# Performance work log

Measured on AMD Instinct MI355X. Metric: run time of the kernel, lower is better.

The kernel has to match this reference:

```python
import jax, jax.numpy as jnp
import numpy as np

N_HEAD = 8
D_HEAD = 128   # dim_k = dim_q = dim_v
SEG_LEN = 512
EPS = 1e-6


def setup_inputs() -> dict:
    key = jax.random.key(0)
    ks = jax.random.split(key, 8)
    B, T, D = 2, 4096, 1024
    scale = 0.02
    x = jax.random.normal(ks[0], (B, T, D), dtype=jnp.float32)
    w_q = jax.random.normal(ks[1], (D, N_HEAD * D_HEAD), dtype=jnp.float32) * scale
    w_k = jax.random.normal(ks[2], (D, N_HEAD * D_HEAD), dtype=jnp.float32) * scale
    w_v = jax.random.normal(ks[3], (D, N_HEAD * D_HEAD), dtype=jnp.float32) * scale
    b_q = jnp.zeros((N_HEAD * D_HEAD,), jnp.float32)
    b_k = jnp.zeros((N_HEAD * D_HEAD,), jnp.float32)
    b_v = jnp.zeros((N_HEAD * D_HEAD,), jnp.float32)
    beta = jnp.zeros((N_HEAD,), jnp.float32)
    return {"x": x, "w_q": w_q, "b_q": b_q, "w_k": w_k, "b_k": b_k,
            "w_v": w_v, "b_v": b_v, "beta": beta}


def _heads(y, B, T):
    # [B,T,H*D] -> [B,H,T,D]
    return y.reshape(B, T, N_HEAD, D_HEAD).transpose(0, 2, 1, 3)


def reference(x, w_q, b_q, w_k, b_k, w_v, b_v, beta):
    B, T, _ = x.shape
    S = T // SEG_LEN
    q = _heads(x @ w_q + b_q, B, T)
    k = _heads(x @ w_k + b_k, B, T)
    v = _heads(x @ w_v + b_v, B, T)

    # segment: [B,H,T,D] -> [S,B,H,L,D]
    def seg(y):
        return y.reshape(B, N_HEAD, S, SEG_LEN, D_HEAD).transpose(2, 0, 1, 3, 4)
    qs, ks_, vs = seg(q), seg(k), seg(v)

    causal = jnp.tril(jnp.ones((SEG_LEN, SEG_LEN), bool))
    gate = jax.nn.sigmoid(beta).reshape(1, N_HEAD, 1, 1)
    inv_sqrt_d = 1.0 / jnp.sqrt(jnp.asarray(D_HEAD, x.dtype))

    def step(carry, segdat):
        M, z = carry                      # M: [B,H,Dk,Dv], z: [B,H,Dk]
        qc, kc, vc = segdat               # [B,H,L,D]
        sq = jax.nn.elu(qc) + 1.0
        sk = jax.nn.elu(kc) + 1.0
        # retrieval from memory BEFORE update
        a_mem = jnp.einsum('bhld,bhde->bhle', sq, M) / (
            jnp.einsum('bhld,bhd->bhl', sq, z)[..., None] + EPS)
        # delta-rule memory update
        retr_k = jnp.einsum('bhld,bhde->bhle', sk, M) / (
            jnp.einsum('bhld,bhd->bhl', sk, z)[..., None] + EPS)
        M = M + jnp.einsum('bhld,bhle->bhde', sk, vc - retr_k)
        z = z + sk.sum(axis=2)
        # local causal dot-product attention within the segment
        scores = jnp.einsum('bhld,bhmd->bhlm', qc, kc) * inv_sqrt_d
        scores = jnp.where(causal, scores, jnp.asarray(-1e30, scores.dtype))
        a_dot = jnp.einsum('bhlm,bhmd->bhld', jax.nn.softmax(scores, axis=-1), vc)
        # long-term context injection
        a = gate * a_mem + (1.0 - gate) * a_dot
        return (M, z), a

    M0 = jnp.zeros((B, N_HEAD, D_HEAD, D_HEAD), x.dtype)
    z0 = jnp.zeros((B, N_HEAD, D_HEAD), x.dtype)
    _, out = jax.lax.scan(step, (M0, z0), (qs, ks_, vs))
    # [S,B,H,L,D] -> [B,T,H*D]
    out = out.transpose(1, 3, 0, 2, 4).reshape(B, T, N_HEAD * D_HEAD)
    # wait: axes of out are [S,B,H,L,D]; reorder to [B,S,L,H,D]
    return out


# fix ordering: define reference properly (overrides above draft path)
def reference(x, w_q, b_q, w_k, b_k, w_v, b_v, beta):
    B, T, _ = x.shape
    S = T // SEG_LEN
    q = _heads(x @ w_q + b_q, B, T)
    k = _heads(x @ w_k + b_k, B, T)
    v = _heads(x @ w_v + b_v, B, T)

    def seg(y):
        return y.reshape(B, N_HEAD, S, SEG_LEN, D_HEAD).transpose(2, 0, 1, 3, 4)
    qs, ks_, vs = seg(q), seg(k), seg(v)

    causal = jnp.tril(jnp.ones((SEG_LEN, SEG_LEN), bool))
    gate = jax.nn.sigmoid(beta).reshape(1, N_HEAD, 1, 1)
    inv_sqrt_d = 1.0 / jnp.sqrt(jnp.asarray(D_HEAD, x.dtype))

    def step(carry, segdat):
        M, z = carry
        qc, kc, vc = segdat
        sq = jax.nn.elu(qc) + 1.0
        sk = jax.nn.elu(kc) + 1.0
        a_mem = jnp.einsum('bhld,bhde->bhle', sq, M) / (
            jnp.einsum('bhld,bhd->bhl', sq, z)[..., None] + EPS)
        retr_k = jnp.einsum('bhld,bhde->bhle', sk, M) / (
            jnp.einsum('bhld,bhd->bhl', sk, z)[..., None] + EPS)
        M = M + jnp.einsum('bhld,bhle->bhde', sk, vc - retr_k)
        z = z + sk.sum(axis=2)
        scores = jnp.einsum('bhld,bhmd->bhlm', qc, kc) * inv_sqrt_d
        scores = jnp.where(causal, scores, jnp.asarray(-1e30, scores.dtype))
        a_dot = jnp.einsum('bhlm,bhmd->bhld', jax.nn.softmax(scores, axis=-1), vc)
        a = gate * a_mem + (1.0 - gate) * a_dot
        return (M, z), a

    M0 = jnp.zeros((B, N_HEAD, D_HEAD, D_HEAD), x.dtype)
    z0 = jnp.zeros((B, N_HEAD, D_HEAD), x.dtype)
    _, out = jax.lax.scan(step, (M0, z0), (qs, ks_, vs))  # [S,B,H,L,D]
    out = out.transpose(1, 0, 3, 2, 4).reshape(B, T, N_HEAD * D_HEAD)
    return out
```

## Files before the change

kernel.cpp:

```cpp
#include <hip/hip_runtime.h>
#include <hip/hip_bf16.h>

typedef __attribute__((ext_vector_type(8))) short bf16x8;
typedef __attribute__((ext_vector_type(4))) float f32x4;
typedef unsigned short u16;
typedef unsigned int u32;

#define DEV static __device__ __forceinline__

DEV float bf2f(u16 u){ u32 x = ((u32)u)<<16; float f; __builtin_memcpy(&f,&x,4); return f; }
DEV u16 f2bf(float f){ u32 x; __builtin_memcpy(&x,&f,4); return (u16)((x + 0x7fffu + ((x>>16)&1u))>>16); }
DEV float elu1(float x){ return x > 0.f ? x + 1.f : __expf(x); }

DEV void gload16(const u16* g, u16* l){
  __builtin_amdgcn_global_load_lds(
      (const __attribute__((address_space(1))) unsigned int*)(g),
      (__attribute__((address_space(3))) unsigned int*)(l), 16, 0, 0);
}

#define MFMA(a,b,c) __builtin_amdgcn_mfma_f32_16x16x32_bf16((a),(b),(c),0,0,0)

#define NB 2
#define NT 4096
#define NH 8
#define DH 128
#define NS 8
#define SL 512
#define ND 1024
#define N3 3072
#define EPS 1e-6f

__global__ __launch_bounds__(256) void k_xc(const float* __restrict__ x, u16* __restrict__ xb){
  int i = blockIdx.x*256 + threadIdx.x;
  const float4 v0 = *(const float4*)(x + (size_t)i*8);
  const float4 v1 = *(const float4*)(x + (size_t)i*8 + 4);
  bf16x8 o;
  o[0]=(short)f2bf(v0.x); o[1]=(short)f2bf(v0.y); o[2]=(short)f2bf(v0.z); o[3]=(short)f2bf(v0.w);
  o[4]=(short)f2bf(v1.x); o[5]=(short)f2bf(v1.y); o[6]=(short)f2bf(v1.z); o[7]=(short)f2bf(v1.w);
  *(bf16x8*)(xb + (size_t)i*8) = o;
}

__global__ __launch_bounds__(256) void k_wt(const float* __restrict__ wq,
                                            const float* __restrict__ wk,
                                            const float* __restrict__ wv,
                                            u16* __restrict__ wt,
                                            float* __restrict__ cs){
  __shared__ float t[32][33];
  const int z = blockIdx.z;
  const float* w = (z==0) ? wq : (z==1 ? wk : wv);
  const int k0 = blockIdx.x*32, n0 = blockIdx.y*32;
  const int tx = threadIdx.x, ty = threadIdx.y;
  if (z==0 && blockIdx.x==0 && blockIdx.y==0){
    const int tid = ty*32 + tx;
#pragma unroll
    for (int i=0;i<64;i++) cs[tid + i*256] = 0.f;
  }
#pragma unroll
  for (int i=0;i<4;i++) t[ty+i*8][tx] = w[(size_t)(k0+ty+i*8)*ND + n0+tx];
  __syncthreads();
#pragma unroll
  for (int i=0;i<4;i++)
    wt[(size_t)(z*ND + n0+ty+i*8)*ND + k0+tx] = f2bf(t[tx][ty+i*8]);
}

__global__ __launch_bounds__(256) void k_gemm(const u16* __restrict__ xb,
                                              const u16* __restrict__ wt,
                                              const float* __restrict__ bq,
                                              const float* __restrict__ bk,
                                              const float* __restrict__ bv,
                                              u16* __restrict__ qkv,
                                              u16* __restrict__ pkTo,
                                              u16* __restrict__ vto,
                                              float* __restrict__ cs){
  __shared__ __align__(16) u16 As[2][128*64];
  __shared__ __align__(16) u16 Bs[2][128*64];
  const int m0 = blockIdx.x*128, n0 = blockIdx.y*128;
  const int tid = threadIdx.x;
  const int w = tid>>6, lane = tid&63, g = lane>>4, li = lane&15;
  const int wr = w>>1, wc = w&1;
  const int srow = lane>>3;
  const int ssl  = (lane&7) ^ srow;
  f32x4 z4 = {0.f,0.f,0.f,0.f};
  f32x4 acc[4][4];
#pragma unroll
  for (int mi=0;mi<4;mi++)
#pragma unroll
    for (int ni=0;ni<4;ni++) acc[mi][ni] = z4;

#define STAGE(kt_) do{                                                          \
    const int k0_ = (kt_)*64;                                                   \
    u16* A_ = (u16*)As[(kt_)&1];                                                \
    u16* B_ = (u16*)Bs[(kt_)&1];                                                \
    _Pragma("unroll")                                                           \
    for (int i_=0;i_<4;i_++){                                                   \
      const int c_ = i_*4 + w;                                                  \
      const int row_ = c_*8 + srow;                                             \
      gload16(xb + (size_t)(m0+row_)*ND + k0_ + ssl*8, A_ + c_*512);            \
      gload16(wt + (size_t)(n0+row_)*ND + k0_ + ssl*8, B_ + c_*512);            \
    }                                                                           \
  }while(0)

  STAGE(0);
  for (int kt=0; kt<16; ++kt){
    if (kt < 15){ STAGE(kt+1); asm volatile("s_waitcnt vmcnt(8)" ::: "memory"); }
    else        {              asm volatile("s_waitcnt vmcnt(0)" ::: "memory"); }
    __builtin_amdgcn_s_barrier();
    __builtin_amdgcn_sched_barrier(0);
    const u16* Ab = (const u16*)As[kt&1];
    const u16* Bb = (const u16*)Bs[kt&1];
#pragma unroll
    for (int kk=0;kk<2;kk++){
      bf16x8 a[4], bb[4];
#pragma unroll
      for (int mi=0;mi<4;mi++){
        int row = wr*64 + mi*16 + li;
        int slot = kk*4 + g;
        a[mi] = *(const bf16x8*)(Ab + row*64 + ((slot^(row&7))<<3));
      }
#pragma unroll
      for (int ni=0;ni<4;ni++){
        int row = wc*64 + ni*16 + li;
        int slot = kk*4 + g;
        bb[ni] = *(const bf16x8*)(Bb + row*64 + ((slot^(row&7))<<3));
      }
#pragma unroll
      for (int mi=0;mi<4;mi++)
#pragma unroll
        for (int ni=0;ni<4;ni++)
          acc[mi][ni] = MFMA(a[mi], bb[ni], acc[mi][ni]);
    }
    __builtin_amdgcn_sched_barrier(0);
    __builtin_amdgcn_s_barrier();
    __builtin_amdgcn_sched_barrier(0);
  }
#undef STAGE

  const int part = n0 >> 10;
  const int hh = (n0 >> 7) & 7;
  const int bb2 = m0 >> 12;
  const int tloc = m0 & (NT-1);
  const int rb = lane>>3, cb = lane&7;
  u16* SCw = (w < 2 ? (u16*)As[0] : (u16*)Bs[0]) + (w&1)*4096;

  if (part < 2){
#pragma unroll
    for (int ni=0;ni<4;ni++){
      const int n = n0 + wc*64 + ni*16 + li;
      const float bias = (part==0) ? bq[n] : bk[n-ND];
#pragma unroll
      for (int mi=0;mi<4;mi++)
#pragma unroll
        for (int rr=0;rr<4;rr++){
          const int ml = mi*16 + 4*g + rr;
          const int nl = ni*16 + li;
          SCw[ml*64 + (((nl>>3)^(ml&7))<<3) + (nl&7)] = f2bf(acc[mi][ni][rr] + bias);
        }
    }
    __syncthreads();
#pragma unroll
    for (int j=0;j<8;j++){
      const int r = j*8 + rb;
      bf16x8 v = *(const bf16x8*)(SCw + r*64 + ((cb^(r&7))<<3));
      *(bf16x8*)(qkv + (size_t)(m0 + wr*64 + r)*N3 + n0 + wc*64 + cb*8) = v;
    }
  }
  if (part >= 1){
    __syncthreads();
    float csum[4] = {0.f,0.f,0.f,0.f};
#pragma unroll
    for (int ni=0;ni<4;ni++){
      const int n = n0 + wc*64 + ni*16 + li;
      const float bias = (part==1) ? bk[n-ND] : bv[n-2*ND];
      const int nl = ni*16 + li;
#pragma unroll
      for (int mi=0;mi<4;mi++){
        float v0 = acc[mi][ni][0] + bias;
        float v1 = acc[mi][ni][1] + bias;
        float v2 = acc[mi][ni][2] + bias;
        float v3 = acc[mi][ni][3] + bias;
        if (part==1){
          v0 = elu1(v0); v1 = elu1(v1); v2 = elu1(v2); v3 = elu1(v3);
          csum[ni] += v0+v1+v2+v3;
        }
        short4 pk;
        pk.x = (short)f2bf(v0); pk.y = (short)f2bf(v1);
        pk.z = (short)f2bf(v2); pk.w = (short)f2bf(v3);
        const int gran = (2*mi + (g>>1)) ^ (nl&7);
        *(short4*)(SCw + nl*64 + (gran<<3) + 4*(g&1)) = pk;
      }
    }
    __syncthreads();
    u16* dstT = (part==1) ? pkTo : vto;
    const int bh = bb2*8 + hh;
#pragma unroll
    for (int j=0;j<8;j++){
      const int r = j*8 + rb;
      bf16x8 v = *(const bf16x8*)(SCw + r*64 + ((cb^(r&7))<<3));
      *(bf16x8*)(dstT + (size_t)(bh*DH + wc*64 + r)*NT + tloc + wr*64 + cb*8) = v;
    }
    if (part==1){
      const int s = tloc >> 9;
      const int bhs = bb2*64 + hh*8 + s;
#pragma unroll
      for (int ni=0;ni<4;ni++){
        float c = csum[ni];
        c += __shfl_xor(c,16); c += __shfl_xor(c,32);
        if (g==0)
          atomicAdd(&cs[(size_t)bhs*DH + wc*64 + ni*16 + li], c);
      }
    }
  }
}

__global__ __launch_bounds__(512) void k_dinv(const u16* __restrict__ qkv,
                                              const float* __restrict__ cs,
                                              float* __restrict__ dinvK){
  const int bhs = blockIdx.x, half = blockIdx.y;
  const int b = bhs>>6, h = (bhs>>3)&7, s = bhs&7;
  const int tid = threadIdx.x, w = tid>>6, lane = tid&63, grp = lane>>4, li = lane&15;
  __shared__ float zl[128];
  if (tid < 128){
    float a = 0.f;
    for (int sp=0; sp<s; ++sp) a += cs[(size_t)(bhs - s + sp)*DH + tid];
    zl[tid] = a;
  }
  __syncthreads();
#pragma unroll
  for (int it=0; it<8; ++it){
    const int r = half*256 + w*32 + it*4 + grp;
    bf16x8 v = *(const bf16x8*)(qkv + (size_t)(b*NT + s*SL + r)*N3 + ND + h*DH + li*8);
    float p = 0.f;
#pragma unroll
    for (int j=0;j<8;j++) p += elu1(bf2f((u16)v[j])) * zl[li*8+j];
    p += __shfl_xor(p,1); p += __shfl_xor(p,2);
    p += __shfl_xor(p,4); p += __shfl_xor(p,8);
    if (li == 0) dinvK[(size_t)bhs*SL + r] = 1.f/(p + EPS);
  }
}

__global__ __launch_bounds__(512) void k_gram(const u16* __restrict__ pkT,
                                              const u16* __restrict__ vtb,
                                              const float* __restrict__ dinvK,
                                              u16* __restrict__ G, float* __restrict__ Bm){
  const int bhs = blockIdx.x, ec = blockIdx.y;
  const int bh = bhs>>3, s = bhs&7, tb = s*SL;
  const int tid = threadIdx.x, w = tid>>6, lane = tid&63, g = lane>>4, li = lane&15;
  __shared__ __align__(16) u16 Bk[32*512];
  __shared__ __align__(16) u16 Bv[32*512];
  __shared__ float dv[512];
  dv[tid] = dinvK[(size_t)bhs*SL + tid];
#pragma unroll
  for (int i=0;i<4;i++){
    const int ee = i*8 + w;
    const size_t rowo = ((size_t)bh*DH + ec*32 + ee)*NT + tb + ((lane^w)<<3);
    gload16(pkT + rowo, Bk + ee*512);
    gload16(vtb + rowo, Bv + ee*512);
  }
  __syncthreads();
  f32x4 z4 = {0.f,0.f,0.f,0.f};
  f32x4 Ga[2] = {z4,z4}, Ba[2] = {z4,z4};
  const u16* arow = pkT + ((size_t)bh*DH + 16*w + li)*NT + tb;
  for (int ks=0; ks<16; ++ks){
    const int r0 = ks*32 + g*8;
    bf16x8 araw = *(const bf16x8*)(arow + r0);
    float4 d0 = *(const float4*)(dv + r0);
    float4 d1 = *(const float4*)(dv + r0 + 4);
    bf16x8 ascl;
    ascl[0] = (short)f2bf(bf2f((u16)araw[0]) * d0.x);
    ascl[1] = (short)f2bf(bf2f((u16)araw[1]) * d0.y);
    ascl[2] = (short)f2bf(bf2f((u16)araw[2]) * d0.z);
    ascl[3] = (short)f2bf(bf2f((u16)araw[3]) * d0.w);
    ascl[4] = (short)f2bf(bf2f((u16)araw[4]) * d1.x);
    ascl[5] = (short)f2bf(bf2f((u16)araw[5]) * d1.y);
    ascl[6] = (short)f2bf(bf2f((u16)araw[6]) * d1.z);
    ascl[7] = (short)f2bf(bf2f((u16)araw[7]) * d1.w);
    const int slot = ks*4 + g;
#pragma unroll
    for (int ni=0;ni<2;ni++){
      const int ee = ni*16 + li;
      bf16x8 bk8 = *(const bf16x8*)(Bk + ee*512 + ((slot^(li&7))<<3));
      bf16x8 bv8 = *(const bf16x8*)(Bv + ee*512 + ((slot^(li&7))<<3));
      Ga[ni] = MFMA(ascl, bk8, Ga[ni]);
      Ba[ni] = MFMA(araw, bv8, Ba[ni]);
    }
  }
#pragma unroll
  for (int ni=0;ni<2;ni++)
#pragma unroll
    for (int rr=0;rr<4;rr++){
      const int dd = 16*w + 4*g + rr;
      const int ee = ec*32 + ni*16 + li;
      G[((size_t)bhs*DH + dd)*DH + ee] = f2bf(Ga[ni][rr]);
      Bm[((size_t)bhs*DH + dd)*DH + ee] = Ba[ni][rr];
    }
}

__global__ __launch_bounds__(512) void k_scan(const u16* __restrict__ G,
                                              const float* __restrict__ Bm,
                                              u16* __restrict__ MTs){
  const int bh = blockIdx.x, ec = blockIdx.y;
  const int tid = threadIdx.x, w = tid>>6, lane = tid&63, g = lane>>4, li = lane&15;
  __shared__ float MF[16*132];
  __shared__ __align__(16) u16 MB[16*128];
  for (int i = tid; i < 16*132; i += 512) MF[i] = 0.f;
  __syncthreads();
  const int dr = w*16 + li;
  for (int s=0;s<NS;s++){
    const size_t bhs = (size_t)bh*NS + s;
    if (tid < 256){
      const int e = tid>>4, dg = tid&15;
      const float* src = MF + e*132 + dg*8;
      bf16x8 v;
#pragma unroll
      for (int j=0;j<8;j++) v[j] = (short)f2bf(src[j]);
      *(bf16x8*)(MTs + bhs*16384 + (size_t)(ec*16+e)*128 + dg*8) = v;
      *(bf16x8*)(MB + e*128 + ((dg^(e&7))<<3)) = v;
    }
    __syncthreads();
    f32x4 acc = {0.f,0.f,0.f,0.f};
#pragma unroll
    for (int ks=0;ks<4;ks++){
      bf16x8 a = *(const bf16x8*)(G + ((size_t)bhs*DH + dr)*DH + ks*32 + g*8);
      const int sl = ks*4 + g;
      bf16x8 bfr = *(const bf16x8*)(MB + li*128 + ((sl^(li&7))<<3));
      acc = MFMA(a, bfr, acc);
    }
#pragma unroll
    for (int rr=0;rr<4;rr++){
      const int d = w*16 + 4*g + rr;
      const float delta = Bm[((size_t)bhs*DH + d)*DH + ec*16 + li] - acc[rr];
      MF[li*132 + d] += delta;
    }
    __syncthreads();
  }
}

__global__ __launch_bounds__(512) void k_attn(const u16* __restrict__ qkv,
                                              const u16* __restrict__ vtb,
                                              const u16* __restrict__ MTs,
                                              const float* __restrict__ cs,
                                              const float* __restrict__ beta,
                                              float* __restrict__ out){
  const int bhs = blockIdx.x, half = blockIdx.y;
  const int b = bhs>>6, h = (bhs>>3)&7, s = bhs&7, bh = bhs>>3;
  const int tid = threadIdx.x, w = tid>>6, lane = tid&63, g = lane>>4, li = lane&15;
  const int jq = (w < 4) ? (half + 2*w) : (15 - half - 2*(w-4));
  const int qb = jq*32;
  const float gate = 1.f/(1.f + __expf(-beta[h]));
  const float SCL = 0.08838834764831845f * 1.4426950408889634f;
  __shared__ __align__(16) u16 P[8*1024];
  __shared__ float zl[128];
  __shared__ float dinvW[8][32];
  u16* Pw = P + w*1024;

  if (tid < 128){
    float a = 0.f;
    for (int sp=0; sp<s; ++sp) a += cs[(size_t)(bhs - s + sp)*DH + tid];
    zl[tid] = a;
  }
  __syncthreads();

  {
    const int r = qb + (lane&31);
    const int dh = (lane>>5)*64;
    const u16* qrow = qkv + (size_t)(b*NT + s*SL + r)*N3 + h*DH + dh;
    float p = 0.f;
#pragma unroll
    for (int j=0;j<64;j+=8){
      bf16x8 v = *(const bf16x8*)(qrow + j);
#pragma unroll
      for (int t=0;t<8;t++) p += elu1(bf2f((u16)v[t])) * zl[dh + j + t];
    }
    p += __shfl_xor(p, 32);
    if (lane < 32) dinvW[w][lane] = 1.f/(p + EPS);
  }

  bf16x8 qf[2][4];
#pragma unroll
  for (int mf=0; mf<2; ++mf)
#pragma unroll
    for (int kf=0; kf<4; ++kf)
      qf[mf][kf] = *(const bf16x8*)(qkv + (size_t)(b*NT + s*SL + qb + mf*16 + li)*N3 + h*DH + kf*32 + g*8);

  bf16x8 one8;
#pragma unroll
  for (int j=0;j<8;j++) one8[j] = (short)0x3F80;

  f32x4 z4 = {0.f,0.f,0.f,0.f};
  f32x4 O[2][8];
  f32x4 lsum[2] = {z4, z4};
#pragma unroll
  for (int mf=0;mf<2;++mf)
#pragma unroll
    for (int nf=0;nf<8;++nf) O[mf][nf] = z4;

  const int nch = jq + 1;
  for (int c=0; c<nch; ++c){
    const int kb = c*32;
    f32x4 sa[2][2];
#pragma unroll
    for (int mf=0;mf<2;++mf)
#pragma unroll
      for (int nf=0;nf<2;++nf) sa[mf][nf] = z4;
#pragma unroll
    for (int kf=0; kf<4; ++kf)
#pragma unroll
      for (int nf=0; nf<2; ++nf){
        bf16x8 bk8 = *(const bf16x8*)(qkv + (size_t)(b*NT + s*SL + kb + nf*16 + li)*N3 + ND + h*DH + kf*32 + g*8);
        sa[0][nf] = MFMA(qf[0][kf], bk8, sa[0][nf]);
        sa[1][nf] = MFMA(qf[1][kf], bk8, sa[1][nf]);
      }
#pragma unroll
    for (int mf=0;mf<2;++mf)
#pragma unroll
      for (int nf=0;nf<2;++nf)
#pragma unroll
        for (int rr=0;rr<4;++rr){
          const int row = qb + mf*16 + 4*g + rr, col = kb + nf*16 + li;
          const float p = (col > row) ? 0.f : exp2f(sa[mf][nf][rr]*SCL);
          const int rl = mf*16 + 4*g + rr, cl = nf*16 + li;
          Pw[rl*32 + (((cl>>3)^(rl&3))<<3) + (cl&7)] = f2bf(p);
        }
    bf16x8 pa[2];
#pragma unroll
    for (int mf=0;mf<2;++mf){
      const int row = mf*16 + li;
      pa[mf] = *(const bf16x8*)(Pw + row*32 + ((g^(row&3))<<3));
    }
#pragma unroll
    for (int nf=0;nf<8;++nf){
      bf16x8 bv8 = *(const bf16x8*)(vtb + ((size_t)bh*DH + nf*16 + li)*NT + s*SL + kb + g*8);
      O[0][nf] = MFMA(pa[0], bv8, O[0][nf]);
      O[1][nf] = MFMA(pa[1], bv8, O[1][nf]);
    }
    lsum[0] = MFMA(pa[0], one8, lsum[0]);
    lsum[1] = MFMA(pa[1], one8, lsum[1]);
  }

  f32x4 Am[2][8];
#pragma unroll
  for (int mf=0;mf<2;++mf)
#pragma unroll
    for (int nf=0;nf<8;++nf) Am[mf][nf] = z4;
#pragma unroll
  for (int ks=0;ks<4;++ks){
    bf16x8 pq[2];
#pragma unroll
    for (int mf=0;mf<2;++mf){
      bf16x8 raw = qf[mf][ks];
#pragma unroll
      for (int j=0;j<8;j++) raw[j] = (short)f2bf(elu1(bf2f((u16)raw[j])));
      pq[mf] = raw;
    }
#pragma unroll
    for (int nf=0;nf<8;++nf){
      bf16x8 bfr = *(const bf16x8*)(MTs + ((size_t)bhs*DH + nf*16 + li)*DH + ks*32 + g*8);
      Am[0][nf] = MFMA(pq[0], bfr, Am[0][nf]);
      Am[1][nf] = MFMA(pq[1], bfr, Am[1][nf]);
    }
  }

  const float og = 1.f - gate;
#pragma unroll
  for (int mf=0;mf<2;++mf)
#pragma unroll
    for (int rr=0;rr<4;++rr){
      const int row = qb + mf*16 + 4*g + rr;
      const float invd = og / lsum[mf][rr];
      const float dv = gate * dinvW[w][row - qb];
#pragma unroll
      for (int nf=0;nf<8;++nf)
        out[(size_t)(b*NT + s*SL + row)*ND + h*DH + nf*16 + li] =
            O[mf][nf][rr]*invd + Am[mf][nf][rr]*dv;
    }
}

extern "C" void kernel_launch(void* const* d_in, const int* in_sizes, int n_in,
                              void* d_out, int out_size, void* d_ws, size_t ws_size,
                              hipStream_t stream) {
  (void)in_sizes; (void)n_in; (void)out_size; (void)ws_size;
  const float* x    = (const float*)d_in[0];
  const float* wq   = (const float*)d_in[1];
  const float* bq   = (const float*)d_in[2];
  const float* wk   = (const float*)d_in[3];
  const float* bk   = (const float*)d_in[4];
  const float* wv   = (const float*)d_in[5];
  const float* bv   = (const float*)d_in[6];
  const float* beta = (const float*)d_in[7];
  float* out = (float*)d_out;
  char* ws = (char*)d_ws;

  u16*   wt  = (u16*)  (ws + 0);
  u16*   qkv = (u16*)  (ws + 6291456);
  u16*   vt  = (u16*)  (ws + 56623104);
  u16*   pkT = (u16*)  (ws + 73400320);
  u16*   G   = (u16*)  (ws + 90177536);
  float* Bm  = (float*)(ws + 94371840);
  u16*   MTs = (u16*)  (ws + 102760448);
  float* cs  = (float*)(ws + 106954752);
  float* dinvK = (float*)(ws + 107020288);
  u16*   xb  = (u16*)  (ws + 90177536);

  hipLaunchKernelGGL(k_xc,    dim3(4096),    dim3(256),  0, stream, x, xb);
  hipLaunchKernelGGL(k_wt,    dim3(32,32,3), dim3(32,8), 0, stream, wq, wk, wv, wt, cs);
  hipLaunchKernelGGL(k_gemm,  dim3(64,24),   dim3(256),  0, stream, xb, wt, bq, bk, bv, qkv, pkT, vt, cs);
  hipLaunchKernelGGL(k_dinv,  dim3(128,2),   dim3(512),  0, stream, qkv, cs, dinvK);
  hipLaunchKernelGGL(k_gram,  dim3(128,4),   dim3(512),  0, stream, pkT, vt, dinvK, G, Bm);
  hipLaunchKernelGGL(k_scan,  dim3(16,8),    dim3(512),  0, stream, G, Bm, MTs);
  hipLaunchKernelGGL(k_attn,  dim3(128,2),   dim3(512),  0, stream, qkv, vt, MTs, cs, beta, out);
}
```

Baseline: 171.7 us.

## Triple-buffer QKV GEMM with BK=32 stages and a single barrier per step

The QKV projection GEMM's K tile shrinks from 64 to 32 and moves from double to triple buffering in LDS, keeping two stages in flight. The loop now needs one barrier per iteration instead of two, and the LDS swizzle changes to match the 32-wide rows. The goal is better overlap of global-to-LDS loads with MFMA work and less synchronisation per step. The trade-off is twice as many iterations with less MFMA work in each, which adds per-iteration overhead.

```diff
diff --git a/kernel.cpp b/kernel.cpp
--- a/kernel.cpp
+++ b/kernel.cpp
@@ -72,14 +72,15 @@
                                               u16* __restrict__ pkTo,
                                               u16* __restrict__ vto,
                                               float* __restrict__ cs){
-  __shared__ __align__(16) u16 As[2][128*64];
-  __shared__ __align__(16) u16 Bs[2][128*64];
+  __shared__ __align__(16) u16 As[3][128*32];
+  __shared__ __align__(16) u16 Bs[3][128*32];
   const int m0 = blockIdx.x*128, n0 = blockIdx.y*128;
   const int tid = threadIdx.x;
   const int w = tid>>6, lane = tid&63, g = lane>>4, li = lane&15;
   const int wr = w>>1, wc = w&1;
-  const int srow = lane>>3;
-  const int ssl  = (lane&7) ^ srow;
+  const int srow2 = lane>>2;
+  const int schk  = (lane&3) ^ (lane>>4);
+  const int rchk  = (li>>2)&3;
   f32x4 z4 = {0.f,0.f,0.f,0.f};
   f32x4 acc[4][4];
 #pragma unroll
@@ -88,49 +89,42 @@
     for (int ni=0;ni<4;ni++) acc[mi][ni] = z4;
 
 #define STAGE(kt_) do{                                                          \
-    const int k0_ = (kt_)*64;                                                   \
-    u16* A_ = (u16*)As[(kt_)&1];                                                \
-    u16* B_ = (u16*)Bs[(kt_)&1];                                                \
+    const int k0_ = (kt_)*32;                                                   \
+    u16* A_ = (u16*)As[(kt_)%3];                                                \
+    u16* B_ = (u16*)Bs[(kt_)%3];                                                \
     _Pragma("unroll")                                                           \
-    for (int i_=0;i_<4;i_++){                                                   \
-      const int c_ = i_*4 + w;                                                  \
-      const int row_ = c_*8 + srow;                                             \
-      gload16(xb + (size_t)(m0+row_)*ND + k0_ + ssl*8, A_ + c_*512);            \
-      gload16(wt + (size_t)(n0+row_)*ND + k0_ + ssl*8, B_ + c_*512);            \
+    for (int j_=0;j_<2;j_++){                                                   \
+      const int r0_ = j_*64 + w*16;                                             \
+      gload16(xb + (size_t)(m0+r0_+srow2)*ND + k0_ + schk*8, A_ + r0_*32);      \
+      gload16(wt + (size_t)(n0+r0_+srow2)*ND + k0_ + schk*8, B_ + r0_*32);      \
     }                                                                           \
   }while(0)
 
-  STAGE(0);
-  for (int kt=0; kt<16; ++kt){
-    if (kt < 15){ STAGE(kt+1); asm volatile("s_waitcnt vmcnt(8)" ::: "memory"); }
-    else        {              asm volatile("s_waitcnt vmcnt(0)" ::: "memory"); }
+  STAGE(0); STAGE(1);
+  for (int kt=0; kt<32; ++kt){
+    if (kt < 31) asm volatile("s_waitcnt vmcnt(4)" ::: "memory");
+    else         asm volatile("s_waitcnt vmcnt(0)" ::: "memory");
     __builtin_amdgcn_s_barrier();
     __builtin_amdgcn_sched_barrier(0);
-    const u16* Ab = (const u16*)As[kt&1];
-    const u16* Bb = (const u16*)Bs[kt&1];
-#pragma unroll
-    for (int kk=0;kk<2;kk++){
-      bf16x8 a[4], bb[4];
-#pragma unroll
-      for (int mi=0;mi<4;mi++){
-        int row = wr*64 + mi*16 + li;
-        int slot = kk*4 + g;
-        a[mi] = *(const bf16x8*)(Ab + row*64 + ((slot^(row&7))<<3));
-      }
-#pragma unroll
-      for (int ni=0;ni<4;ni++){
-        int row = wc*64 + ni*16 + li;
-        int slot = kk*4 + g;
-        bb[ni] = *(const bf16x8*)(Bb + row*64 + ((slot^(row&7))<<3));
-      }
-#pragma unroll
-      for (int mi=0;mi<4;mi++)
-#pragma unroll
-        for (int ni=0;ni<4;ni++)
-          acc[mi][ni] = MFMA(a[mi], bb[ni], acc[mi][ni]);
-    }
-    __builtin_amdgcn_sched_barrier(0);
-    __builtin_amdgcn_s_barrier();
+    if (kt < 30) STAGE(kt+2);
+    const u16* Ab = (const u16*)As[kt%3];
+    const u16* Bb = (const u16*)Bs[kt%3];
+    bf16x8 a[4], bb[4];
+#pragma unroll
+    for (int mi=0;mi<4;mi++){
+      const int row = wr*64 + mi*16 + li;
+      a[mi] = *(const bf16x8*)(Ab + row*32 + ((g^rchk)<<3));
+    }
+#pragma unroll
+    for (int ni=0;ni<4;ni++){
+      const int row = wc*64 + ni*16 + li;
+      bb[ni] = *(const bf16x8*)(Bb + row*32 + ((g^rchk)<<3));
+    }
+#pragma unroll
+    for (int mi=0;mi<4;mi++)
+#pragma unroll
+      for (int ni=0;ni<4;ni++)
+        acc[mi][ni] = MFMA(a[mi], bb[ni], acc[mi][ni]);
     __builtin_amdgcn_sched_barrier(0);
   }
 #undef STAGE
```

After: 188.2 us. 1.1x slower.
